# Kernel tuning notes

Hardware: AMD Instinct MI355X
Metric: run time of the kernel (lower is better)

The kernel has to match this reference:

```python
import jax, jax.numpy as jnp
import numpy as np

NEG_SLOPE = 0.2


def setup_inputs() -> dict:
    key = jax.random.key(0)
    k1, k2, k3, k4, k5 = jax.random.split(key, 5)
    N, F_in, F_out, H, D = 4096, 256, 256, 4, 64
    x = jax.random.normal(k1, (N, F_in), dtype=jnp.float32)
    adj = jax.random.normal(k2, (N, N), dtype=jnp.float32)  # ~half entries > 0 -> edges
    W = jax.random.normal(k3, (F_out, F_in), dtype=jnp.float32) * (1.0 / np.sqrt(F_in))
    a_src = jax.random.normal(k4, (H, D), dtype=jnp.float32) * 0.1
    a_dst = jax.random.normal(k5, (H, D), dtype=jnp.float32) * 0.1
    return {"x": x, "adj": adj, "W": W, "a_src": a_src, "a_dst": a_dst}


def reference(x, adj, W, a_src, a_dst):
    N = x.shape[0]
    H, D = a_src.shape
    # linear projection (torch Linear: x @ W.T), reshape to heads
    h = (x @ W.T).reshape(N, H, D)                      # [N, H, D]
    attn_src = jnp.einsum('nhd,hd->nh', h, a_src)       # [N, H]
    attn_dst = jnp.einsum('nhd,hd->nh', h, a_dst)       # [N, H]
    scores = attn_src[:, None, :] + attn_dst[None, :, :]  # [N, N, H]
    scores = jnp.where(scores >= 0, scores, NEG_SLOPE * scores)  # leaky_relu(0.2)
    mask = (adj > 0)[:, :, None]                        # [N, N, 1]
    scores = jnp.where(mask, scores, -jnp.inf)
    attn = jax.nn.softmax(scores, axis=1)               # softmax over neighbors j
    attn = jnp.nan_to_num(attn, nan=0.0)                # fully-masked rows -> 0
    weighted = attn * adj[:, :, None]                   # weight by adjacency values
    out = jnp.einsum('ijh,jhd->ihd', weighted, h)       # [N, H, D]
    return out.reshape(N, H * D)
```

## Files before the change

### kernel.cpp

```cpp
#include <hip/hip_runtime.h>
#include <stdint.h>

#define NN 4096
#define FF 256
#define HH 4
#define DD 64
#define NEG 0.2f
#define LOG2E 1.4426950408889634f

#define ITILE 32
#define CJ 64

typedef __attribute__((ext_vector_type(8))) short short8;
typedef __attribute__((ext_vector_type(4))) float f32x4;
typedef __attribute__((ext_vector_type(16))) float f32x16;

__device__ __forceinline__ uint16_t bf16_rh(float f) {
    uint32_t u = __float_as_uint(f);
    return (uint16_t)((u + 0x8000u) >> 16);
}

__global__ __launch_bounds__(256) void cvt_inputs(const float* __restrict__ x,
                                                  const float* __restrict__ W,
                                                  uint16_t* __restrict__ xb,
                                                  uint16_t* __restrict__ Wb,
                                                  float4* __restrict__ pden4) {
    const int idx = blockIdx.x * 256 + threadIdx.x;
    const int nx = NN * FF / 4;
    const int nw = FF * FF / 4;
    if (idx < NN * HH / 4) pden4[idx] = make_float4(0.f, 0.f, 0.f, 0.f);
    if (idx < nx) {
        float4 v = ((const float4*)x)[idx];
        ushort4 o;
        o.x = bf16_rh(v.x); o.y = bf16_rh(v.y);
        o.z = bf16_rh(v.z); o.w = bf16_rh(v.w);
        ((ushort4*)xb)[idx] = o;
    } else if (idx < nx + nw) {
        int k = idx - nx;
        float4 v = ((const float4*)W)[k];
        ushort4 o;
        o.x = bf16_rh(v.x); o.y = bf16_rh(v.y);
        o.z = bf16_rh(v.z); o.w = bf16_rh(v.w);
        ((ushort4*)Wb)[k] = o;
    }
}

__global__ __launch_bounds__(256) void gemm_h(const uint16_t* __restrict__ xb,
                                              const uint16_t* __restrict__ Wb,
                                              const float* __restrict__ a_src,
                                              const float* __restrict__ a_dst,
                                              float* __restrict__ s,
                                              float* __restrict__ T_T,
                                              uint16_t* __restrict__ H_T) {
    const int tid = threadIdx.x;
    const int w = tid >> 6, l = tid & 63;
    const int m = l & 15, q = l >> 4;
    const int i0 = blockIdx.x * 64 + w * 16;
    const int f0 = blockIdx.y * 64;
    const int hh = blockIdx.y;
    f32x4 acc[4];
#pragma unroll
    for (int n = 0; n < 4; n++)
#pragma unroll
        for (int r = 0; r < 4; r++) acc[n][r] = 0.f;
    const uint16_t* arow = xb + (size_t)(i0 + m) * FF + q * 8;
#pragma unroll
    for (int k0 = 0; k0 < FF; k0 += 32) {
        short8 af = *(const short8*)(arow + k0);
#pragma unroll
        for (int n = 0; n < 4; n++) {
            short8 bf = *(const short8*)(Wb + (size_t)(f0 + n * 16 + m) * FF + k0 + q * 8);
            acc[n] = __builtin_amdgcn_mfma_f32_16x16x32_bf16(af, bf, acc[n], 0, 0, 0);
        }
    }
    const float* as = a_src + hh * DD;
    const float* ad = a_dst + hh * DD;
    float av[4], dv[4];
#pragma unroll
    for (int n = 0; n < 4; n++) { av[n] = as[n * 16 + m]; dv[n] = ad[n * 16 + m]; }
#pragma unroll
    for (int r = 0; r < 4; r++) {
        float vs = 0.f, vd = 0.f;
#pragma unroll
        for (int n = 0; n < 4; n++) {
            vs = fmaf(acc[n][r], av[n], vs);
            vd = fmaf(acc[n][r], dv[n], vd);
        }
#pragma unroll
        for (int off = 1; off < 16; off <<= 1) {
            vs += __shfl_xor(vs, off, 64);
            vd += __shfl_xor(vd, off, 64);
        }
        if (m == 0) {
            const int i = i0 + q * 4 + r;
            s[(size_t)i * HH + hh] = vs * LOG2E;
            T_T[(size_t)hh * NN + i] = vd * LOG2E;
        }
    }
#pragma unroll
    for (int n = 0; n < 4; n++) {
        ushort4 o;
        o.x = bf16_rh(acc[n][0]); o.y = bf16_rh(acc[n][1]);
        o.z = bf16_rh(acc[n][2]); o.w = bf16_rh(acc[n][3]);
        *(ushort4*)(H_T + (size_t)(f0 + n * 16 + m) * NN + i0 + q * 4) = o;
    }
}

template<int NS>
__global__ __launch_bounds__(256, 4) void gat_main(
    const float* __restrict__ adj, const uint16_t* __restrict__ H_T,
    const float* __restrict__ s, const float* __restrict__ T_T,
    float* __restrict__ pden, uint16_t* __restrict__ part) {
    constexpr int JR = NN / NS;
    __shared__ float adj_s[CJ][ITILE + 1];
    const int tid = threadIdx.x;
    const int w = tid >> 6, l = tid & 63;
    const int m = l & 31, q = l >> 5;
    constexpr int NWG = (NN / ITILE) * NS;
    const int orig = blockIdx.y * (NN / ITILE) + blockIdx.x;
    const int swz = (orig & 7) * (NWG / 8) + (orig >> 3);
    const int i0 = (swz & (NN / ITILE - 1)) * ITILE;
    const int sl = swz / (NN / ITILE);
    const int jb = sl * JR;

    const float sS = s[(size_t)(i0 + m) * HH + w];
    const float sB = NEG * sS;
    float den = 0.f;
    f32x16 acc0, acc1;
#pragma unroll
    for (int r = 0; r < 16; r++) { acc0[r] = 0.f; acc1[r] = 0.f; }
    const float* trow = T_T + (size_t)w * NN;
    const uint16_t* b0row = H_T + (size_t)(w * DD + m) * NN;
    const uint16_t* b1row = H_T + (size_t)(w * DD + 32 + m) * NN;

    const int is = tid >> 3, j8 = (tid & 7) * 8;
    const float* arow = adj + (size_t)(i0 + is) * NN + j8;
    float4 pre0 = *(const float4*)(arow + jb);
    float4 pre1 = *(const float4*)(arow + jb + 4);

    for (int jc = jb; jc < jb + JR; jc += CJ) {
        __syncthreads();
        adj_s[j8 + 0][is] = pre0.x; adj_s[j8 + 1][is] = pre0.y;
        adj_s[j8 + 2][is] = pre0.z; adj_s[j8 + 3][is] = pre0.w;
        adj_s[j8 + 4][is] = pre1.x; adj_s[j8 + 5][is] = pre1.y;
        adj_s[j8 + 6][is] = pre1.z; adj_s[j8 + 7][is] = pre1.w;
        if (jc + CJ < jb + JR) {
            pre0 = *(const float4*)(arow + jc + CJ);
            pre1 = *(const float4*)(arow + jc + CJ + 4);
        }
        __syncthreads();
#pragma unroll
        for (int kk = 0; kk < CJ; kk += 16) {
            const int jg = jc + kk + q * 8;
            float4 t0 = *(const float4*)(trow + jg);
            float4 t1 = *(const float4*)(trow + jg + 4);
            float tt[8] = {t0.x, t0.y, t0.z, t0.w, t1.x, t1.y, t1.z, t1.w};
            uint32_t pk[4];
#pragma unroll
            for (int jj = 0; jj < 8; jj += 2) {
                float av0 = adj_s[kk + q * 8 + jj][m];
                float av1 = adj_s[kk + q * 8 + jj + 1][m];
                float x10 = sS + tt[jj],     x20 = fmaf(NEG, tt[jj], sB);
                float x11 = sS + tt[jj + 1], x21 = fmaf(NEG, tt[jj + 1], sB);
                float lr0 = fmaxf(x10, x20), lr1 = fmaxf(x11, x21);
                float e0, e1;
                asm("v_exp_f32 %0, %1" : "=v"(e0) : "v"(lr0));
                asm("v_exp_f32 %0, %1" : "=v"(e1) : "v"(lr1));
                e0 = (av0 > 0.f) ? e0 : 0.f;
                e1 = (av1 > 0.f) ? e1 : 0.f;
                den += e0 + e1;
                float p0 = e0 * av0, p1 = e1 * av1;
                uint32_t u0 = __float_as_uint(p0) + 0x8000u;
                uint32_t u1 = __float_as_uint(p1) + 0x8000u;
                pk[jj >> 1] = (u0 >> 16) | (u1 & 0xffff0000u);
            }
            union { uint32_t u[4]; short8 v; } afu;
#pragma unroll
            for (int c = 0; c < 4; c++) afu.u[c] = pk[c];
            short8 bf0 = *(const short8*)(b0row + jg);
            short8 bf1 = *(const short8*)(b1row + jg);
            acc0 = __builtin_amdgcn_mfma_f32_32x32x16_bf16(afu.v, bf0, acc0, 0, 0, 0);
            acc1 = __builtin_amdgcn_mfma_f32_32x32x16_bf16(afu.v, bf1, acc1, 0, 0, 0);
        }
    }
    den += __shfl_down(den, 32, 64);
    if (l < 32) atomicAdd(&pden[(size_t)(i0 + m) * HH + w], den);
    uint16_t* pbase = part + (size_t)sl * NN * FF;
#pragma unroll
    for (int reg = 0; reg < 16; reg++) {
        int row = (reg & 3) + 8 * (reg >> 2) + 4 * q;
        pbase[(size_t)(i0 + row) * FF + w * DD + m]      = bf16_rh(acc0[reg]);
        pbase[(size_t)(i0 + row) * FF + w * DD + 32 + m] = bf16_rh(acc1[reg]);
    }
}

template<int NS>
__global__ __launch_bounds__(256) void finalize(const uint16_t* __restrict__ part,
                                                const float* __restrict__ pden,
                                                float* __restrict__ out) {
    const int i = blockIdx.x, f = threadIdx.x;
    float sum = 0.f;
#pragma unroll
    for (int sl = 0; sl < NS; sl++) {
        uint16_t v = part[(size_t)sl * NN * FF + (size_t)i * FF + f];
        sum += __uint_as_float(((uint32_t)v) << 16);
    }
    float d = pden[(size_t)i * HH + (f >> 6)];
    out[(size_t)i * FF + f] = (d > 0.f) ? sum / d : 0.f;
}

extern "C" void kernel_launch(void* const* d_in, const int* in_sizes, int n_in,
                              void* d_out, int out_size, void* d_ws, size_t ws_size,
                              hipStream_t stream) {
    const float* x     = (const float*)d_in[0];
    const float* adj   = (const float*)d_in[1];
    const float* W     = (const float*)d_in[2];
    const float* a_src = (const float*)d_in[3];
    const float* a_dst = (const float*)d_in[4];
    float* out = (float*)d_out;

    char* ws = (char*)d_ws;
    uint16_t* H_T  = (uint16_t*)ws;
    uint16_t* xb   = (uint16_t*)(ws + (2u << 20));
    uint16_t* Wb   = (uint16_t*)(ws + (4u << 20));
    float*    s    = (float*)(ws + (4u << 20) + (128u << 10));
    float*    T_T  = s + (size_t)NN * HH;
    float*    pden = T_T + (size_t)HH * NN;
    uint16_t* part = (uint16_t*)(ws + (5u << 20));

    cvt_inputs<<<(NN * FF / 4 + FF * FF / 4 + 255) / 256, 256, 0, stream>>>(
        x, W, xb, Wb, (float4*)pden);
    gemm_h<<<dim3(NN / 64, FF / 64), 256, 0, stream>>>(xb, Wb, a_src, a_dst, s, T_T, H_T);
    if (ws_size >= (5u << 20) + (size_t)16 * NN * FF * sizeof(uint16_t)) {
        gat_main<16><<<dim3(NN / ITILE, 16), 256, 0, stream>>>(adj, H_T, s, T_T, pden, part);
        finalize<16><<<NN, 256, 0, stream>>>(part, pden, out);
    } else {
        gat_main<8><<<dim3(NN / ITILE, 8), 256, 0, stream>>>(adj, H_T, s, T_T, pden, part);
        finalize<8><<<NN, 256, 0, stream>>>(part, pden, out);
    }
}
```

Before: 161.8 us.

## Widen GAT row tile to 64, double-buffer adj, fuse conversion into GEMM

The main attention kernel now covers 64 rows per block, so each H_T B-fragment and T row load feeds two sets of MFMAs. The adjacency tile is double-buffered in shared memory so there is one barrier per chunk instead of two. The separate bf16 conversion kernel is removed: gemm_h converts x and W on the fly and also zeroes pden. finalize is vectorized to four outputs per thread. The cost is more accumulator registers (occupancy hint lowered to 3) and half as many blocks in gat_main.

```diff
diff --git a/kernel.cpp b/kernel.cpp
--- a/kernel.cpp
+++ b/kernel.cpp
@@ -8,7 +8,7 @@
 #define NEG 0.2f
 #define LOG2E 1.4426950408889634f
 
-#define ITILE 32
+#define ITILE 64
 #define CJ 64
 
 typedef __attribute__((ext_vector_type(8))) short short8;
@@ -19,40 +19,30 @@
     uint32_t u = __float_as_uint(f);
     return (uint16_t)((u + 0x8000u) >> 16);
 }
-
-__global__ __launch_bounds__(256) void cvt_inputs(const float* __restrict__ x,
-                                                  const float* __restrict__ W,
-                                                  uint16_t* __restrict__ xb,
-                                                  uint16_t* __restrict__ Wb,
-                                                  float4* __restrict__ pden4) {
-    const int idx = blockIdx.x * 256 + threadIdx.x;
-    const int nx = NN * FF / 4;
-    const int nw = FF * FF / 4;
-    if (idx < NN * HH / 4) pden4[idx] = make_float4(0.f, 0.f, 0.f, 0.f);
-    if (idx < nx) {
-        float4 v = ((const float4*)x)[idx];
-        ushort4 o;
-        o.x = bf16_rh(v.x); o.y = bf16_rh(v.y);
-        o.z = bf16_rh(v.z); o.w = bf16_rh(v.w);
-        ((ushort4*)xb)[idx] = o;
-    } else if (idx < nx + nw) {
-        int k = idx - nx;
-        float4 v = ((const float4*)W)[k];
-        ushort4 o;
-        o.x = bf16_rh(v.x); o.y = bf16_rh(v.y);
-        o.z = bf16_rh(v.z); o.w = bf16_rh(v.w);
-        ((ushort4*)Wb)[k] = o;
-    }
-}
-
-__global__ __launch_bounds__(256) void gemm_h(const uint16_t* __restrict__ xb,
-                                              const uint16_t* __restrict__ Wb,
+__device__ __forceinline__ uint32_t pk2(float a, float b) {
+    uint32_t ua = __float_as_uint(a) + 0x8000u;
+    uint32_t ub = __float_as_uint(b) + 0x8000u;
+    return (ua >> 16) | (ub & 0xffff0000u);
+}
+__device__ __forceinline__ short8 ld_bf8(const float* __restrict__ p) {
+    float4 v0 = *(const float4*)p;
+    float4 v1 = *(const float4*)(p + 4);
+    union { uint32_t u[4]; short8 v; } o;
+    o.u[0] = pk2(v0.x, v0.y); o.u[1] = pk2(v0.z, v0.w);
+    o.u[2] = pk2(v1.x, v1.y); o.u[3] = pk2(v1.z, v1.w);
+    return o.v;
+}
+
+__global__ __launch_bounds__(256) void gemm_h(const float* __restrict__ x,
+                                              const float* __restrict__ W,
                                               const float* __restrict__ a_src,
                                               const float* __restrict__ a_dst,
                                               float* __restrict__ s,
                                               float* __restrict__ T_T,
-                                              uint16_t* __restrict__ H_T) {
+                                              uint16_t* __restrict__ H_T,
+                                              float* __restrict__ pden) {
     const int tid = threadIdx.x;
+    if (blockIdx.y == 0) pden[blockIdx.x * 256 + tid] = 0.f;
     const int w = tid >> 6, l = tid & 63;
     const int m = l & 15, q = l >> 4;
     const int i0 = blockIdx.x * 64 + w * 16;
@@ -63,13 +53,13 @@
     for (int n = 0; n < 4; n++)
 #pragma unroll
         for (int r = 0; r < 4; r++) acc[n][r] = 0.f;
-    const uint16_t* arow = xb + (size_t)(i0 + m) * FF + q * 8;
+    const float* arow = x + (size_t)(i0 + m) * FF + q * 8;
 #pragma unroll
     for (int k0 = 0; k0 < FF; k0 += 32) {
-        short8 af = *(const short8*)(arow + k0);
+        short8 af = ld_bf8(arow + k0);
 #pragma unroll
         for (int n = 0; n < 4; n++) {
-            short8 bf = *(const short8*)(Wb + (size_t)(f0 + n * 16 + m) * FF + k0 + q * 8);
+            short8 bf = ld_bf8(W + (size_t)(f0 + n * 16 + m) * FF + k0 + q * 8);
             acc[n] = __builtin_amdgcn_mfma_f32_16x16x32_bf16(af, bf, acc[n], 0, 0, 0);
         }
     }
@@ -107,12 +97,13 @@
 }
 
 template<int NS>
-__global__ __launch_bounds__(256, 4) void gat_main(
+__global__ __launch_bounds__(256, 3) void gat_main(
     const float* __restrict__ adj, const uint16_t* __restrict__ H_T,
     const float* __restrict__ s, const float* __restrict__ T_T,
     float* __restrict__ pden, uint16_t* __restrict__ part) {
     constexpr int JR = NN / NS;
-    __shared__ float adj_s[CJ][ITILE + 1];
+    constexpr int NCH = JR / CJ;
+    __shared__ float adj_s[2][CJ][ITILE + 1];
     const int tid = threadIdx.x;
     const int w = tid >> 6, l = tid & 63;
     const int m = l & 31, q = l >> 5;
@@ -123,74 +114,112 @@
     const int sl = swz / (NN / ITILE);
     const int jb = sl * JR;
 
-    const float sS = s[(size_t)(i0 + m) * HH + w];
-    const float sB = NEG * sS;
-    float den = 0.f;
-    f32x16 acc0, acc1;
-#pragma unroll
-    for (int r = 0; r < 16; r++) { acc0[r] = 0.f; acc1[r] = 0.f; }
+    const float sA = s[(size_t)(i0 + m) * HH + w];
+    const float sB = s[(size_t)(i0 + 32 + m) * HH + w];
+    const float cA = NEG * sA, cB = NEG * sB;
+    float denA = 0.f, denB = 0.f;
+    f32x16 acc0a, acc1a, acc0b, acc1b;
+#pragma unroll
+    for (int r = 0; r < 16; r++) {
+        acc0a[r] = 0.f; acc1a[r] = 0.f; acc0b[r] = 0.f; acc1b[r] = 0.f;
+    }
     const float* trow = T_T + (size_t)w * NN;
     const uint16_t* b0row = H_T + (size_t)(w * DD + m) * NN;
     const uint16_t* b1row = H_T + (size_t)(w * DD + 32 + m) * NN;
 
-    const int is = tid >> 3, j8 = (tid & 7) * 8;
-    const float* arow = adj + (size_t)(i0 + is) * NN + j8;
-    float4 pre0 = *(const float4*)(arow + jb);
-    float4 pre1 = *(const float4*)(arow + jb + 4);
-
-    for (int jc = jb; jc < jb + JR; jc += CJ) {
-        __syncthreads();
-        adj_s[j8 + 0][is] = pre0.x; adj_s[j8 + 1][is] = pre0.y;
-        adj_s[j8 + 2][is] = pre0.z; adj_s[j8 + 3][is] = pre0.w;
-        adj_s[j8 + 4][is] = pre1.x; adj_s[j8 + 5][is] = pre1.y;
-        adj_s[j8 + 6][is] = pre1.z; adj_s[j8 + 7][is] = pre1.w;
-        if (jc + CJ < jb + JR) {
-            pre0 = *(const float4*)(arow + jc + CJ);
-            pre1 = *(const float4*)(arow + jc + CJ + 4);
-        }
-        __syncthreads();
+    const int is = tid >> 2, j16 = (tid & 3) * 16;
+    const float* arow = adj + (size_t)(i0 + is) * NN + j16;
+
+    float4 pre[4];
+#pragma unroll
+    for (int c4 = 0; c4 < 4; c4++) pre[c4] = *(const float4*)(arow + jb + c4 * 4);
+#pragma unroll
+    for (int c4 = 0; c4 < 4; c4++) {
+        adj_s[0][j16 + c4 * 4 + 0][is] = pre[c4].x;
+        adj_s[0][j16 + c4 * 4 + 1][is] = pre[c4].y;
+        adj_s[0][j16 + c4 * 4 + 2][is] = pre[c4].z;
+        adj_s[0][j16 + c4 * 4 + 3][is] = pre[c4].w;
+    }
+#pragma unroll
+    for (int c4 = 0; c4 < 4; c4++) pre[c4] = *(const float4*)(arow + jb + CJ + c4 * 4);
+    __syncthreads();
+
+    for (int c = 0; c < NCH; ++c) {
+        const int jc = jb + c * CJ;
+        const int cur = c & 1;
+        if (c + 1 < NCH) {
+#pragma unroll
+            for (int c4 = 0; c4 < 4; c4++) {
+                adj_s[cur ^ 1][j16 + c4 * 4 + 0][is] = pre[c4].x;
+                adj_s[cur ^ 1][j16 + c4 * 4 + 1][is] = pre[c4].y;
+                adj_s[cur ^ 1][j16 + c4 * 4 + 2][is] = pre[c4].z;
+                adj_s[cur ^ 1][j16 + c4 * 4 + 3][is] = pre[c4].w;
+            }
+            if (c + 2 < NCH) {
+#pragma unroll
+                for (int c4 = 0; c4 < 4; c4++)
+                    pre[c4] = *(const float4*)(arow + jc + 2 * CJ + c4 * 4);
+            }
+        }
 #pragma unroll
         for (int kk = 0; kk < CJ; kk += 16) {
             const int jg = jc + kk + q * 8;
             float4 t0 = *(const float4*)(trow + jg);
             float4 t1 = *(const float4*)(trow + jg + 4);
             float tt[8] = {t0.x, t0.y, t0.z, t0.w, t1.x, t1.y, t1.z, t1.w};
-            uint32_t pk[4];
+            uint32_t pka[4], pkb[4];
 #pragma unroll
             for (int jj = 0; jj < 8; jj += 2) {
-                float av0 = adj_s[kk + q * 8 + jj][m];
-                float av1 = adj_s[kk + q * 8 + jj + 1][m];
-                float x10 = sS + tt[jj],     x20 = fmaf(NEG, tt[jj], sB);
-                float x11 = sS + tt[jj + 1], x21 = fmaf(NEG, tt[jj + 1], sB);
-                float lr0 = fmaxf(x10, x20), lr1 = fmaxf(x11, x21);
-                float e0, e1;
-                asm("v_exp_f32 %0, %1" : "=v"(e0) : "v"(lr0));
-                asm("v_exp_f32 %0, %1" : "=v"(e1) : "v"(lr1));
-                e0 = (av0 > 0.f) ? e0 : 0.f;
-                e1 = (av1 > 0.f) ? e1 : 0.f;
-                den += e0 + e1;
-                float p0 = e0 * av0, p1 = e1 * av1;
-                uint32_t u0 = __float_as_uint(p0) + 0x8000u;
-                uint32_t u1 = __float_as_uint(p1) + 0x8000u;
-                pk[jj >> 1] = (u0 >> 16) | (u1 & 0xffff0000u);
+                const int rr = kk + q * 8 + jj;
+                float a0A = adj_s[cur][rr][m],      a1A = adj_s[cur][rr + 1][m];
+                float a0B = adj_s[cur][rr][m + 32], a1B = adj_s[cur][rr + 1][m + 32];
+                float tv0 = tt[jj], tv1 = tt[jj + 1];
+                float y0 = NEG * tv0, y1 = NEG * tv1;
+                float xa0 = sA + tv0, xa1 = sA + tv1;
+                float la0 = fmaxf(xa0, y0 + cA), la1 = fmaxf(xa1, y1 + cA);
+                float ea0, ea1;
+                asm("v_exp_f32 %0, %1" : "=v"(ea0) : "v"(la0));
+                asm("v_exp_f32 %0, %1" : "=v"(ea1) : "v"(la1));
+                ea0 = (a0A > 0.f) ? ea0 : 0.f;
+                ea1 = (a1A > 0.f) ? ea1 : 0.f;
+                denA += ea0 + ea1;
+                pka[jj >> 1] = pk2(ea0 * a0A, ea1 * a1A);
+                float xb0 = sB + tv0, xb1 = sB + tv1;
+                float lb0 = fmaxf(xb0, y0 + cB), lb1 = fmaxf(xb1, y1 + cB);
+                float eb0, eb1;
+                asm("v_exp_f32 %0, %1" : "=v"(eb0) : "v"(lb0));
+                asm("v_exp_f32 %0, %1" : "=v"(eb1) : "v"(lb1));
+                eb0 = (a0B > 0.f) ? eb0 : 0.f;
+                eb1 = (a1B > 0.f) ? eb1 : 0.f;
+                denB += eb0 + eb1;
+                pkb[jj >> 1] = pk2(eb0 * a0B, eb1 * a1B);
             }
-            union { uint32_t u[4]; short8 v; } afu;
-#pragma unroll
-            for (int c = 0; c < 4; c++) afu.u[c] = pk[c];
+            union { uint32_t u[4]; short8 v; } ua, ub;
+#pragma unroll
+            for (int c4 = 0; c4 < 4; c4++) { ua.u[c4] = pka[c4]; ub.u[c4] = pkb[c4]; }
             short8 bf0 = *(const short8*)(b0row + jg);
             short8 bf1 = *(const short8*)(b1row + jg);
-            acc0 = __builtin_amdgcn_mfma_f32_32x32x16_bf16(afu.v, bf0, acc0, 0, 0, 0);
-            acc1 = __builtin_amdgcn_mfma_f32_32x32x16_bf16(afu.v, bf1, acc1, 0, 0, 0);
-        }
-    }
-    den += __shfl_down(den, 32, 64);
-    if (l < 32) atomicAdd(&pden[(size_t)(i0 + m) * HH + w], den);
+            acc0a = __builtin_amdgcn_mfma_f32_32x32x16_bf16(ua.v, bf0, acc0a, 0, 0, 0);
+            acc1a = __builtin_amdgcn_mfma_f32_32x32x16_bf16(ua.v, bf1, acc1a, 0, 0, 0);
+            acc0b = __builtin_amdgcn_mfma_f32_32x32x16_bf16(ub.v, bf0, acc0b, 0, 0, 0);
+            acc1b = __builtin_amdgcn_mfma_f32_32x32x16_bf16(ub.v, bf1, acc1b, 0, 0, 0);
+        }
+        __syncthreads();
+    }
+    denA += __shfl_down(denA, 32, 64);
+    denB += __shfl_down(denB, 32, 64);
+    if (l < 32) {
+        atomicAdd(&pden[(size_t)(i0 + m) * HH + w], denA);
+        atomicAdd(&pden[(size_t)(i0 + 32 + m) * HH + w], denB);
+    }
     uint16_t* pbase = part + (size_t)sl * NN * FF;
 #pragma unroll
     for (int reg = 0; reg < 16; reg++) {
         int row = (reg & 3) + 8 * (reg >> 2) + 4 * q;
-        pbase[(size_t)(i0 + row) * FF + w * DD + m]      = bf16_rh(acc0[reg]);
-        pbase[(size_t)(i0 + row) * FF + w * DD + 32 + m] = bf16_rh(acc1[reg]);
+        pbase[(size_t)(i0 + row) * FF + w * DD + m]           = bf16_rh(acc0a[reg]);
+        pbase[(size_t)(i0 + row) * FF + w * DD + 32 + m]      = bf16_rh(acc1a[reg]);
+        pbase[(size_t)(i0 + 32 + row) * FF + w * DD + m]      = bf16_rh(acc0b[reg]);
+        pbase[(size_t)(i0 + 32 + row) * FF + w * DD + 32 + m] = bf16_rh(acc1b[reg]);
     }
 }
 
@@ -198,15 +227,21 @@
 __global__ __launch_bounds__(256) void finalize(const uint16_t* __restrict__ part,
                                                 const float* __restrict__ pden,
                                                 float* __restrict__ out) {
-    const int i = blockIdx.x, f = threadIdx.x;
-    float sum = 0.f;
+    const int i = blockIdx.x * 4 + (threadIdx.x >> 6);
+    const int fq = (threadIdx.x & 63) * 4;
+    float s0 = 0.f, s1 = 0.f, s2 = 0.f, s3 = 0.f;
 #pragma unroll
     for (int sl = 0; sl < NS; sl++) {
-        uint16_t v = part[(size_t)sl * NN * FF + (size_t)i * FF + f];
-        sum += __uint_as_float(((uint32_t)v) << 16);
-    }
-    float d = pden[(size_t)i * HH + (f >> 6)];
-    out[(size_t)i * FF + f] = (d > 0.f) ? sum / d : 0.f;
+        ushort4 v = *(const ushort4*)(part + (size_t)sl * NN * FF + (size_t)i * FF + fq);
+        s0 += __uint_as_float(((uint32_t)v.x) << 16);
+        s1 += __uint_as_float(((uint32_t)v.y) << 16);
+        s2 += __uint_as_float(((uint32_t)v.z) << 16);
+        s3 += __uint_as_float(((uint32_t)v.w) << 16);
+    }
+    float d = pden[(size_t)i * HH + (fq >> 6)];
+    float inv = (d > 0.f) ? 1.f / d : 0.f;
+    *(float4*)(out + (size_t)i * FF + fq) =
+        make_float4(s0 * inv, s1 * inv, s2 * inv, s3 * inv);
 }
 
 extern "C" void kernel_launch(void* const* d_in, const int* in_sizes, int n_in,
@@ -221,21 +256,17 @@
 
     char* ws = (char*)d_ws;
     uint16_t* H_T  = (uint16_t*)ws;
-    uint16_t* xb   = (uint16_t*)(ws + (2u << 20));
-    uint16_t* Wb   = (uint16_t*)(ws + (4u << 20));
-    float*    s    = (float*)(ws + (4u << 20) + (128u << 10));
+    float*    s    = (float*)(ws + (2u << 20));
     float*    T_T  = s + (size_t)NN * HH;
     float*    pden = T_T + (size_t)HH * NN;
-    uint16_t* part = (uint16_t*)(ws + (5u << 20));
-
-    cvt_inputs<<<(NN * FF / 4 + FF * FF / 4 + 255) / 256, 256, 0, stream>>>(
-        x, W, xb, Wb, (float4*)pden);
-    gemm_h<<<dim3(NN / 64, FF / 64), 256, 0, stream>>>(xb, Wb, a_src, a_dst, s, T_T, H_T);
-    if (ws_size >= (5u << 20) + (size_t)16 * NN * FF * sizeof(uint16_t)) {
+    uint16_t* part = (uint16_t*)(ws + (3u << 20));
+
+    gemm_h<<<dim3(NN / 64, HH), 256, 0, stream>>>(x, W, a_src, a_dst, s, T_T, H_T, pden);
+    if (ws_size >= (3u << 20) + (size_t)16 * NN * FF * sizeof(uint16_t)) {
         gat_main<16><<<dim3(NN / ITILE, 16), 256, 0, stream>>>(adj, H_T, s, T_T, pden, part);
-        finalize<16><<<NN, 256, 0, stream>>>(part, pden, out);
+        finalize<16><<<NN / 4, 256, 0, stream>>>(part, pden, out);
     } else {
         gat_main<8><<<dim3(NN / ITILE, 8), 256, 0, stream>>>(adj, H_T, s, T_T, pden, part);
-        finalize<8><<<NN, 256, 0, stream>>>(part, pden, out);
-    }
-}
+        finalize<8><<<NN / 4, 256, 0, stream>>>(part, pden, out);
+    }
+}
```

Measured after the change: 182.8 us. 1.13x slower.
